# Optimization experiments

Measured on AMD Instinct MI355X. Metric: run time of the kernel, lower is better.

Reference implementation:

```python
import jax, jax.numpy as jnp
import numpy as np

N_STATIONS = 100000
N_TIME = 365
N_NEIGHBORS = 5
SMOOTHING = 0.1


def setup_inputs() -> dict:
    key = jax.random.key(0)
    k = jax.random.split(key, 6)
    N, T, K = N_STATIONS, N_TIME, N_NEIGHBORS
    time_vector = jnp.arange(T, dtype=jnp.float32) / 365.25  # years
    constant_offset = jax.random.normal(k[0], (N,), jnp.float32) * 10.0
    linear_trend = jax.random.normal(k[1], (N,), jnp.float32) * 5.0  # mm/yr (ps00_rates buffer)
    seasonal_amplitudes = jax.random.uniform(k[2], (N, 4), jnp.float32) * 6.0
    seasonal_phases = jax.random.uniform(k[3], (N, 4), jnp.float32) * (2.0 * np.pi)
    neighbor_indices = jax.random.randint(k[4], (N, K), 0, N)
    w = jax.random.uniform(k[5], (N, K), jnp.float32) + 1e-3
    neighbor_weights = w / jnp.sum(w, axis=1, keepdims=True)  # row-normalized, like exp-dist weights
    periods = jnp.array([0.25, 0.5, 1.0, 2.0], dtype=jnp.float32)
    return {
        'time_vector': time_vector,
        'constant_offset': constant_offset,
        'linear_trend': linear_trend,
        'seasonal_amplitudes': seasonal_amplitudes,
        'seasonal_phases': seasonal_phases,
        'neighbor_weights': neighbor_weights,
        'periods': periods,
        'neighbor_indices': neighbor_indices,
    }


def _smooth(p, neighbor_indices, neighbor_weights):
    # p: [N, 4]; vectorized version of per-station loop: gather + weighted mean
    nb = p[neighbor_indices]                                   # [N, K, 4]
    avg = jnp.einsum('nkf,nk->nf', nb, neighbor_weights)       # [N, 4]
    return (1.0 - SMOOTHING) * p + SMOOTHING * avg


def reference(time_vector, constant_offset, linear_trend, seasonal_amplitudes,
              seasonal_phases, neighbor_weights, periods, neighbor_indices):
    amps = _smooth(seasonal_amplitudes, neighbor_indices, neighbor_weights)   # [N, 4]
    phs = _smooth(seasonal_phases, neighbor_indices, neighbor_weights)        # [N, 4]
    t = time_vector[None, :]                                                  # [1, T]
    signals = constant_offset[:, None] + linear_trend[:, None] * t           # [N, T]
    two_pi = jnp.float32(2.0 * np.pi)
    for f in range(4):  # fixed small set of seasonal periods
        freq = 1.0 / periods[f]
        signals = signals + amps[:, f:f + 1] * jnp.sin(two_pi * freq * t + phs[:, f:f + 1])
    return signals
```

## Files before the change

### kernel.cpp

```cpp
#include <hip/hip_runtime.h>
#include <math.h>

typedef float f32x2 __attribute__((ext_vector_type(2)));

#define TWO_PI 6.283185307179586f
#define SMOOTH 0.1f
#define SPW 8
#define WAVES 4
#define BLOCK 256
#define SPB (SPW * WAVES)
#define NPAIR 3
#define HROWS 4

__device__ __forceinline__ f32x2 sp2(float x) { f32x2 r; r.x = x; r.y = x; return r; }
__device__ __forceinline__ float rlane(float v, int l) {
    return __uint_as_float((unsigned)__builtin_amdgcn_readlane((int)__float_as_uint(v), l));
}

__global__ __launch_bounds__(BLOCK) void fused_v7(
    const float* __restrict__ time_vector,
    const float* __restrict__ constant_offset,
    const float* __restrict__ linear_trend,
    const float* __restrict__ amps,
    const float* __restrict__ phs,
    const float* __restrict__ wgt,
    const float* __restrict__ periods,
    const int*   __restrict__ nbidx,
    float* __restrict__ out,
    int N, int T, int K)
{
    extern __shared__ float lds[];

    const int tid   = threadIdx.x;
    const int wave  = tid >> 6;
    const int lane  = tid & 63;
    const int wbase = blockIdx.x * SPB + wave * SPW;

    if (wbase >= N) return;
    int send = N - wbase; if (send > SPW) send = SPW;

    int sid = wbase + (lane & (SPW - 1));
    if (sid >= N) sid = N - 1;

    float4 a = reinterpret_cast<const float4*>(amps)[sid];
    float4 p = reinterpret_cast<const float4*>(phs)[sid];

    int   nb[5]; float w[5];
    __builtin_memcpy(nb, nbidx + (size_t)sid * K, 5 * sizeof(int));
    __builtin_memcpy(w,  wgt   + (size_t)sid * K, 5 * sizeof(float));

    float av0 = 0.f, av1 = 0.f, av2 = 0.f, av3 = 0.f;
    float pv0 = 0.f, pv1 = 0.f, pv2 = 0.f, pv3 = 0.f;
    #pragma unroll
    for (int k = 0; k < 5; ++k) {
        float4 na = reinterpret_cast<const float4*>(amps)[nb[k]];
        float4 np = reinterpret_cast<const float4*>(phs)[nb[k]];
        av0 += w[k] * na.x; av1 += w[k] * na.y; av2 += w[k] * na.z; av3 += w[k] * na.w;
        pv0 += w[k] * np.x; pv1 += w[k] * np.y; pv2 += w[k] * np.z; pv3 += w[k] * np.w;
    }
    float sa0 = (1.0f - SMOOTH) * a.x + SMOOTH * av0;
    float sa1 = (1.0f - SMOOTH) * a.y + SMOOTH * av1;
    float sa2 = (1.0f - SMOOTH) * a.z + SMOOTH * av2;
    float sa3 = (1.0f - SMOOTH) * a.w + SMOOTH * av3;
    float sp0 = (1.0f - SMOOTH) * p.x + SMOOTH * pv0;
    float sp1 = (1.0f - SMOOTH) * p.y + SMOOTH * pv1;
    float sp2v = (1.0f - SMOOTH) * p.z + SMOOTH * pv2;
    float sp3 = (1.0f - SMOOTH) * p.w + SMOOTH * pv3;

    float cc = constant_offset[sid];
    float cm = linear_trend[sid];
    float cA0 = sa0 * __cosf(sp0),  cB0 = sa0 * __sinf(sp0);
    float cA1 = sa1 * __cosf(sp1),  cB1 = sa1 * __sinf(sp1);
    float cA2 = sa2 * __cosf(sp2v), cB2 = sa2 * __sinf(sp2v);
    float cA3 = sa3 * __cosf(sp3),  cB3 = sa3 * __sinf(sp3);

    const float w0 = TWO_PI / periods[0];
    const float w1 = TWO_PI / periods[1];
    const float w2 = TWO_PI / periods[2];
    const float w3 = TWO_PI / periods[3];

    f32x2 tv[NPAIR];
    f32x2 bs[NPAIR][4], bc[NPAIR][4];
    bool full[NPAIR], any[NPAIR];
    const int t0 = 2 * lane;

    #pragma unroll
    for (int q = 0; q < NPAIR; ++q) {
        const int t = t0 + 128 * q;
        const bool v0 = (t < T), v1 = (t + 1 < T);
        any[q] = v0; full[q] = v1;
        float ta = v0 ? time_vector[t]     : 0.f;
        float tb = v1 ? time_vector[t + 1] : 0.f;
        f32x2 tvp; tvp.x = ta; tvp.y = tb;
        tv[q] = tvp;
        #pragma unroll
        for (int f = 0; f < 4; ++f) {
            const float wf = (f == 0) ? w0 : (f == 1) ? w1 : (f == 2) ? w2 : w3;
            f32x2 s, c;
            s.x = __sinf(wf * ta); s.y = __sinf(wf * tb);
            c.x = __cosf(wf * ta); c.y = __cosf(wf * tb);
            bs[q][f] = s; bc[q][f] = c;
        }
    }

    float* wlds = lds + (size_t)wave * HROWS * T;

    if (send == SPW) {
        #pragma unroll
        for (int half = 0; half < 2; ++half) {
            #pragma unroll
            for (int j4 = 0; j4 < HROWS; ++j4) {
                const int j = half * HROWS + j4;
                float sc  = rlane(cc,  j), sm  = rlane(cm,  j);
                float sA0 = rlane(cA0, j), sB0 = rlane(cB0, j);
                float sA1 = rlane(cA1, j), sB1 = rlane(cB1, j);
                float sA2 = rlane(cA2, j), sB2 = rlane(cB2, j);
                float sA3 = rlane(cA3, j), sB3 = rlane(cB3, j);
                float* lrow = wlds + j4 * T;

                #pragma unroll
                for (int q = 0; q < NPAIR; ++q) {
                    f32x2 sig = sp2(sc) + sp2(sm) * tv[q];
                    sig += sp2(sA0) * bs[q][0] + sp2(sB0) * bc[q][0];
                    sig += sp2(sA1) * bs[q][1] + sp2(sB1) * bc[q][1];
                    sig += sp2(sA2) * bs[q][2] + sp2(sB2) * bc[q][2];
                    sig += sp2(sA3) * bs[q][3] + sp2(sB3) * bc[q][3];
                    const int t = t0 + 128 * q;
                    if (full[q]) { lrow[t] = sig.x; lrow[t + 1] = sig.y; }
                    else if (any[q]) { lrow[t] = sig.x; }
                }
            }
            __builtin_amdgcn_sched_barrier(0);
            __builtin_amdgcn_wave_barrier();

            const float4* src = reinterpret_cast<const float4*>(wlds);
            float4* dst = reinterpret_cast<float4*>(
                out + ((size_t)wbase + half * HROWS) * T);
            const int nch = T;
            for (int it = lane; it < nch; it += 64)
                dst[it] = src[it];

            __builtin_amdgcn_sched_barrier(0);
            __builtin_amdgcn_wave_barrier();
        }
    } else {
        float* obase = out + (size_t)wbase * T;
        for (int j = 0; j < send; ++j) {
            float sc  = rlane(cc,  j), sm  = rlane(cm,  j);
            float sA0 = rlane(cA0, j), sB0 = rlane(cB0, j);
            float sA1 = rlane(cA1, j), sB1 = rlane(cB1, j);
            float sA2 = rlane(cA2, j), sB2 = rlane(cB2, j);
            float sA3 = rlane(cA3, j), sB3 = rlane(cB3, j);
            float* orow = obase + (size_t)j * T;
            #pragma unroll
            for (int q = 0; q < NPAIR; ++q) {
                f32x2 sig = sp2(sc) + sp2(sm) * tv[q];
                sig += sp2(sA0) * bs[q][0] + sp2(sB0) * bc[q][0];
                sig += sp2(sA1) * bs[q][1] + sp2(sB1) * bc[q][1];
                sig += sp2(sA2) * bs[q][2] + sp2(sB2) * bc[q][2];
                sig += sp2(sA3) * bs[q][3] + sp2(sB3) * bc[q][3];
                const int t = t0 + 128 * q;
                if (full[q]) { orow[t] = sig.x; orow[t + 1] = sig.y; }
                else if (any[q]) { orow[t] = sig.x; }
            }
        }
    }
}

extern "C" void kernel_launch(void* const* d_in, const int* in_sizes, int n_in,
                              void* d_out, int out_size, void* d_ws, size_t ws_size,
                              hipStream_t stream)
{
    const float* time_vector     = (const float*)d_in[0];
    const float* constant_offset = (const float*)d_in[1];
    const float* linear_trend    = (const float*)d_in[2];
    const float* amps            = (const float*)d_in[3];
    const float* phs             = (const float*)d_in[4];
    const float* wgt             = (const float*)d_in[5];
    const float* periods         = (const float*)d_in[6];
    const int*   nbidx           = (const int*)d_in[7];

    int T = in_sizes[0];
    int N = in_sizes[1];
    int K = in_sizes[5] / N;
    float* out = (float*)d_out;

    int grid = (N + SPB - 1) / SPB;
    size_t shmem = (size_t)WAVES * HROWS * T * sizeof(float);
    fused_v7<<<grid, BLOCK, shmem, stream>>>(
        time_vector, constant_offset, linear_trend, amps, phs, wgt,
        periods, nbidx, out, N, T, K);
}
```

Before: 40.41 us.

## Stage whole block's output rows in LDS and copy out with block-wide stores

Each wave now writes all 8 of its station rows into a block-sized LDS slab instead of two 4-row halves. After a __syncthreads, all 256 threads copy the block's contiguous 32-row region to global memory with float4 stores. The aim is longer contiguous write streams and fewer per-wave staging rounds. In exchange LDS use doubles to about 46KB per block, which may limit occupancy, and a block-wide barrier replaces the wave-local sync.

```diff
diff --git a/kernel.cpp b/kernel.cpp
--- a/kernel.cpp
+++ b/kernel.cpp
@@ -10,14 +10,13 @@
 #define BLOCK 256
 #define SPB (SPW * WAVES)
 #define NPAIR 3
-#define HROWS 4
 
 __device__ __forceinline__ f32x2 sp2(float x) { f32x2 r; r.x = x; r.y = x; return r; }
 __device__ __forceinline__ float rlane(float v, int l) {
     return __uint_as_float((unsigned)__builtin_amdgcn_readlane((int)__float_as_uint(v), l));
 }
 
-__global__ __launch_bounds__(BLOCK) void fused_v7(
+__global__ __launch_bounds__(BLOCK) void fused_v9(
     const float* __restrict__ time_vector,
     const float* __restrict__ constant_offset,
     const float* __restrict__ linear_trend,
@@ -29,15 +28,16 @@
     float* __restrict__ out,
     int N, int T, int K)
 {
-    extern __shared__ float lds[];
+    extern __shared__ float slab[];
 
-    const int tid   = threadIdx.x;
-    const int wave  = tid >> 6;
-    const int lane  = tid & 63;
-    const int wbase = blockIdx.x * SPB + wave * SPW;
+    const int tid    = threadIdx.x;
+    const int wave   = tid >> 6;
+    const int lane   = tid & 63;
+    const int bbase  = blockIdx.x * SPB;
+    const int wbase  = bbase + wave * SPW;
 
-    if (wbase >= N) return;
-    int send = N - wbase; if (send > SPW) send = SPW;
+    if (bbase >= N) return;
+    int bsend = N - bbase; if (bsend > SPB) bsend = SPB;
 
     int sid = wbase + (lane & (SPW - 1));
     if (sid >= N) sid = N - 1;
@@ -103,47 +103,41 @@
         }
     }
 
-    float* wlds = lds + (size_t)wave * HROWS * T;
+    if (bsend == SPB) {
+        float* wrows = slab + (size_t)(wave * SPW) * T;
 
-    if (send == SPW) {
         #pragma unroll
-        for (int half = 0; half < 2; ++half) {
+        for (int j = 0; j < SPW; ++j) {
+            float sc  = rlane(cc,  j), sm  = rlane(cm,  j);
+            float sA0 = rlane(cA0, j), sB0 = rlane(cB0, j);
+            float sA1 = rlane(cA1, j), sB1 = rlane(cB1, j);
+            float sA2 = rlane(cA2, j), sB2 = rlane(cB2, j);
+            float sA3 = rlane(cA3, j), sB3 = rlane(cB3, j);
+            float* lrow = wrows + (size_t)j * T;
+
             #pragma unroll
-            for (int j4 = 0; j4 < HROWS; ++j4) {
-                const int j = half * HROWS + j4;
-                float sc  = rlane(cc,  j), sm  = rlane(cm,  j);
-                float sA0 = rlane(cA0, j), sB0 = rlane(cB0, j);
-                float sA1 = rlane(cA1, j), sB1 = rlane(cB1, j);
-                float sA2 = rlane(cA2, j), sB2 = rlane(cB2, j);
-                float sA3 = rlane(cA3, j), sB3 = rlane(cB3, j);
-                float* lrow = wlds + j4 * T;
+            for (int q = 0; q < NPAIR; ++q) {
+                f32x2 sig = sp2(sc) + sp2(sm) * tv[q];
+                sig += sp2(sA0) * bs[q][0] + sp2(sB0) * bc[q][0];
+                sig += sp2(sA1) * bs[q][1] + sp2(sB1) * bc[q][1];
+                sig += sp2(sA2) * bs[q][2] + sp2(sB2) * bc[q][2];
+                sig += sp2(sA3) * bs[q][3] + sp2(sB3) * bc[q][3];
+                const int t = t0 + 128 * q;
+                if (full[q]) { lrow[t] = sig.x; lrow[t + 1] = sig.y; }
+                else if (any[q]) { lrow[t] = sig.x; }
+            }
+        }
 
-                #pragma unroll
-                for (int q = 0; q < NPAIR; ++q) {
-                    f32x2 sig = sp2(sc) + sp2(sm) * tv[q];
-                    sig += sp2(sA0) * bs[q][0] + sp2(sB0) * bc[q][0];
-                    sig += sp2(sA1) * bs[q][1] + sp2(sB1) * bc[q][1];
-                    sig += sp2(sA2) * bs[q][2] + sp2(sB2) * bc[q][2];
-                    sig += sp2(sA3) * bs[q][3] + sp2(sB3) * bc[q][3];
-                    const int t = t0 + 128 * q;
-                    if (full[q]) { lrow[t] = sig.x; lrow[t + 1] = sig.y; }
-                    else if (any[q]) { lrow[t] = sig.x; }
-                }
-            }
-            __builtin_amdgcn_sched_barrier(0);
-            __builtin_amdgcn_wave_barrier();
+        __syncthreads();
 
-            const float4* src = reinterpret_cast<const float4*>(wlds);
-            float4* dst = reinterpret_cast<float4*>(
-                out + ((size_t)wbase + half * HROWS) * T);
-            const int nch = T;
-            for (int it = lane; it < nch; it += 64)
-                dst[it] = src[it];
-
-            __builtin_amdgcn_sched_barrier(0);
-            __builtin_amdgcn_wave_barrier();
-        }
+        const float4* lsrc = reinterpret_cast<const float4*>(slab);
+        float4* gdst = reinterpret_cast<float4*>(out + (size_t)bbase * T);
+        const int nch = (SPB * T) >> 2;
+        for (int i = tid; i < nch; i += BLOCK)
+            gdst[i] = lsrc[i];
     } else {
+        int send = N - wbase; if (send > SPW) send = SPW;
+        if (send <= 0) return;
         float* obase = out + (size_t)wbase * T;
         for (int j = 0; j < send; ++j) {
             float sc  = rlane(cc,  j), sm  = rlane(cm,  j);
@@ -186,8 +180,8 @@
     float* out = (float*)d_out;
 
     int grid = (N + SPB - 1) / SPB;
-    size_t shmem = (size_t)WAVES * HROWS * T * sizeof(float);
-    fused_v7<<<grid, BLOCK, shmem, stream>>>(
+    size_t shmem = (size_t)SPB * T * sizeof(float);
+    fused_v9<<<grid, BLOCK, shmem, stream>>>(
         time_vector, constant_offset, linear_trend, amps, phs, wgt,
         periods, nbidx, out, N, T, K);
 }
```

After: 41.60 us. +3.0%, slower.
